# Optimization experiments

Hardware: AMD Instinct MI355X
Metric: run time of the kernel (lower is better)

Reference implementation:

```python
import jax, jax.numpy as jnp
import numpy as np

WS = 7
NHEAD = 8


def setup_inputs() -> dict:
    key = jax.random.key(0)
    k1, k2, k3 = jax.random.split(key, 3)
    B, H, W, D = 32, 56, 56, 256
    x = jax.random.normal(k1, (B, H, W, D), dtype=jnp.float32)
    in_proj_w = jax.random.normal(k2, (3 * D, D), dtype=jnp.float32) * 0.02
    in_proj_b = jnp.zeros((3 * D,), dtype=jnp.float32)
    out_w = jax.random.normal(k3, (D, D), dtype=jnp.float32) * 0.02
    out_b = jnp.zeros((D,), dtype=jnp.float32)
    return {"x": x, "in_proj_w": in_proj_w, "in_proj_b": in_proj_b,
            "out_w": out_w, "out_b": out_b}


def reference(x, in_proj_w, in_proj_b, out_w, out_b):
    B, Hf, Wf, D = x.shape
    ws = WS
    hd = D // NHEAD
    pad_h = (-Hf) % ws
    pad_w = (-Wf) % ws
    xp = jnp.pad(x, ((0, 0), (0, pad_h), (0, pad_w), (0, 0)))
    Hp, Wp = Hf + pad_h, Wf + pad_w
    nh, nw = Hp // ws, Wp // ws
    # partition into windows: [B*nh*nw, ws*ws, D]
    xw = xp.reshape(B, nh, ws, nw, ws, D).transpose(0, 1, 3, 2, 4, 5)
    xw = xw.reshape(B * nh * nw, ws * ws, D)
    N, L = xw.shape[0], ws * ws
    # qkv projection (torch MHA: x @ in_proj_w.T + in_proj_b)
    qkv = jnp.einsum('nld,ed->nle', xw, in_proj_w) + in_proj_b  # [N, L, 3D]
    q, k, v = jnp.split(qkv, 3, axis=-1)
    q = q.reshape(N, L, NHEAD, hd).transpose(0, 2, 1, 3)
    k = k.reshape(N, L, NHEAD, hd).transpose(0, 2, 1, 3)
    v = v.reshape(N, L, NHEAD, hd).transpose(0, 2, 1, 3)
    scale = 1.0 / np.sqrt(hd).astype(np.float32)
    scores = jnp.einsum('nhqd,nhkd->nhqk', q * scale, k)  # [N, H, L, L]
    attn = jax.nn.softmax(scores, axis=-1)
    o = jnp.einsum('nhqk,nhkd->nhqd', attn, v)
    o = o.transpose(0, 2, 1, 3).reshape(N, L, D)
    o = jnp.einsum('nld,ed->nle', o, out_w) + out_b
    # un-window
    o = o.reshape(B, nh, nw, ws, ws, D).transpose(0, 1, 3, 2, 4, 5)
    o = o.reshape(B, Hp, Wp, D)
    return o[:, :Hf, :Wf, :]
```

## Files before the change

kernel.cpp:

```cpp
#include <hip/hip_runtime.h>


using f16   = _Float16;
using f16x4 = __attribute__((ext_vector_type(4))) _Float16;
using f16x8 = __attribute__((ext_vector_type(8))) _Float16;
using f32x4 = __attribute__((ext_vector_type(4))) float;

#define NTOK   100352
#define DMODEL 256
#define QKVN   768
#define LDSK   72

typedef const __attribute__((address_space(1))) unsigned int* as1_u32p;
typedef __attribute__((address_space(3))) unsigned int* as3_u32p;

__device__ __forceinline__ void gload16(const void* g, void* l) {
    __builtin_amdgcn_global_load_lds((as1_u32p)g, (as3_u32p)l, 16, 0, 0);
}

__device__ __forceinline__ f16x8 zero8() {
    f16x8 z;
#pragma unroll
    for (int i = 0; i < 8; ++i) z[i] = (f16)0;
    return z;
}

#define XV4   6422528
#define WQV4  49152
__global__ __launch_bounds__(256) void convert_all(
    const float* __restrict__ X, const float* __restrict__ Wq,
    f16* __restrict__ Xh, f16* __restrict__ Wqh)
{
    const float scale = 0.17677669529663687f;
    const int total = XV4 + WQV4;
    for (int i = blockIdx.x * blockDim.x + threadIdx.x; i < total;
         i += gridDim.x * blockDim.x) {
        float4 f;
        f16x4 h;
        if (i < XV4) {
            f = reinterpret_cast<const float4*>(X)[i];
            h[0]=(f16)f.x; h[1]=(f16)f.y; h[2]=(f16)f.z; h[3]=(f16)f.w;
            reinterpret_cast<f16x4*>(Xh)[i] = h;
        } else {
            int idx = i - XV4;
            int row = idx >> 6;
            float sc = (row < 256) ? scale : 1.0f;
            f = reinterpret_cast<const float4*>(Wq)[idx];
            h[0]=(f16)(f.x*sc); h[1]=(f16)(f.y*sc); h[2]=(f16)(f.z*sc); h[3]=(f16)(f.w*sc);
            reinterpret_cast<f16x4*>(Wqh)[idx] = h;
        }
    }
}

__global__ __launch_bounds__(256) void qkv_gemm(
    const f16* __restrict__ Xh,
    const f16* __restrict__ Wh,
    const float* __restrict__ bias,
    f16* __restrict__ QKV)
{
    __shared__ f16 As[128 * 64];
    __shared__ f16 Bs[128 * 64];
    const int tid  = threadIdx.x;
    const int lane = tid & 63;
    const int wave = tid >> 6;
    int wg = blockIdx.x;
    const int cpx = (NTOK / 128) * (QKVN / 128) / 8;
    wg = (wg & 7) * cpx + (wg >> 3);
    const int m0 = (wg / (QKVN / 128)) * 128;
    const int n0 = (wg % (QKVN / 128)) * 128;
    const int wm = (wave >> 1) * 64;
    const int wn = (wave & 1) * 64;
    const int g  = lane >> 4;
    const int lr = lane & 15;

    f32x4 acc[4][4] = {};

    for (int k0 = 0; k0 < 256; k0 += 64) {
#pragma unroll
        for (int j = 0; j < 4; ++j) {
            int s   = wave * 64 + lane + j * 256;
            int row = s >> 3;
            int cs  = (s & 7) ^ (row & 7);
            gload16(Xh + (size_t)(m0 + row) * 256 + k0 + cs * 8,
                    &As[(size_t)(wave * 64 + j * 256) * 8]);
            gload16(Wh + (size_t)(n0 + row) * 256 + k0 + cs * 8,
                    &Bs[(size_t)(wave * 64 + j * 256) * 8]);
        }
        __syncthreads();
#pragma unroll
        for (int ks = 0; ks < 2; ++ks) {
            f16x8 a[4], b[4];
#pragma unroll
            for (int i = 0; i < 4; ++i) {
                int row = wm + i * 16 + lr;
                int c   = ((ks << 2) + g) ^ (row & 7);
                a[i] = *reinterpret_cast<const f16x8*>(&As[row * 64 + c * 8]);
            }
#pragma unroll
            for (int i = 0; i < 4; ++i) {
                int row = wn + i * 16 + lr;
                int c   = ((ks << 2) + g) ^ (row & 7);
                b[i] = *reinterpret_cast<const f16x8*>(&Bs[row * 64 + c * 8]);
            }
#pragma unroll
            for (int mi = 0; mi < 4; ++mi)
#pragma unroll
                for (int ni = 0; ni < 4; ++ni)
                    acc[mi][ni] = __builtin_amdgcn_mfma_f32_16x16x32_f16(a[mi], b[ni], acc[mi][ni], 0, 0, 0);
        }
        __syncthreads();
    }
    const float scale = 0.17677669529663687f;
#pragma unroll
    for (int ni = 0; ni < 4; ++ni) {
        int n = n0 + wn + ni * 16 + lr;
        float bv = bias[n];
        if (n < 256) bv *= scale;
#pragma unroll
        for (int mi = 0; mi < 4; ++mi)
#pragma unroll
            for (int r = 0; r < 4; ++r) {
                int m = m0 + wm + mi * 16 + g * 4 + r;
                QKV[(size_t)m * QKVN + n] = (f16)(acc[mi][ni][r] + bv);
            }
    }
}

__global__ __launch_bounds__(64) void win_attn(f16* __restrict__ QKV)
{
    __shared__ f16 Vt[32][LDSK];
    __shared__ f16 P[64][LDSK];
    const int lane = threadIdx.x;
    const int widx = blockIdx.x;
    const int win = widx >> 3, h = widx & 7;
    const int b = win >> 6, wh = (win >> 3) & 7, ww = win & 7;
    const int base = (b * 56 + wh * 7) * 56 + ww * 7;
    const int g = lane >> 4, lr = lane & 15;

    auto tok = [&](int row) { int rr = row / 7; return base + rr * 56 + (row - rr * 7); };

    f16x8 qf[4], kf[4];
#pragma unroll
    for (int i = 0; i < 4; ++i) {
        int row = i * 16 + lr;
        if (row < 49) {
            size_t off = (size_t)tok(row) * QKVN + h * 32 + g * 8;
            qf[i] = *reinterpret_cast<const f16x8*>(QKV + off);
            kf[i] = *reinterpret_cast<const f16x8*>(QKV + off + 256);
        } else { qf[i] = zero8(); kf[i] = zero8(); }
    }
    {
        int kk = lane;
        if (kk < 49) {
            size_t off = (size_t)tok(kk) * QKVN + 512 + h * 32;
            f16x8 vv[4];
#pragma unroll
            for (int j = 0; j < 4; ++j)
                vv[j] = *reinterpret_cast<const f16x8*>(QKV + off + j * 8);
#pragma unroll
            for (int j = 0; j < 4; ++j)
#pragma unroll
                for (int d = 0; d < 8; ++d) Vt[j * 8 + d][kk] = vv[j][d];
        } else {
#pragma unroll
            for (int d = 0; d < 32; ++d) Vt[d][kk] = (f16)0;
        }
    }
    f32x4 s[4][4] = {};
#pragma unroll
    for (int mi = 0; mi < 4; ++mi)
#pragma unroll
        for (int ni = 0; ni < 4; ++ni)
            s[mi][ni] = __builtin_amdgcn_mfma_f32_16x16x32_f16(qf[mi], kf[ni], s[mi][ni], 0, 0, 0);

    __syncthreads();
#pragma unroll
    for (int mi = 0; mi < 4; ++mi) {
#pragma unroll
        for (int r = 0; r < 4; ++r) {
            float vals[4];
            float mx = -1e30f;
#pragma unroll
            for (int ni = 0; ni < 4; ++ni) {
                int col = ni * 16 + lr;
                vals[ni] = s[mi][ni][r];
                if (col < 49) mx = fmaxf(mx, vals[ni]);
            }
#pragma unroll
            for (int d = 8; d >= 1; d >>= 1) mx = fmaxf(mx, __shfl_xor(mx, d, 64));
            float p[4], sum = 0.f;
#pragma unroll
            for (int ni = 0; ni < 4; ++ni) {
                int col = ni * 16 + lr;
                p[ni] = (col < 49) ? __expf(vals[ni] - mx) : 0.f;
                sum += p[ni];
            }
#pragma unroll
            for (int d = 8; d >= 1; d >>= 1) sum += __shfl_xor(sum, d, 64);
            float is = 1.f / sum;
            int row = mi * 16 + g * 4 + r;
#pragma unroll
            for (int ni = 0; ni < 4; ++ni)
                P[row][ni * 16 + lr] = (f16)(p[ni] * is);
        }
    }
    __syncthreads();

    f32x4 o[4][2] = {};
#pragma unroll
    for (int ks = 0; ks < 2; ++ks) {
        f16x8 pa[4], vb[2];
#pragma unroll
        for (int mi = 0; mi < 4; ++mi)
            pa[mi] = *reinterpret_cast<const f16x8*>(&P[mi * 16 + lr][ks * 32 + g * 8]);
#pragma unroll
        for (int ni = 0; ni < 2; ++ni)
            vb[ni] = *reinterpret_cast<const f16x8*>(&Vt[ni * 16 + lr][ks * 32 + g * 8]);
#pragma unroll
        for (int mi = 0; mi < 4; ++mi)
#pragma unroll
            for (int ni = 0; ni < 2; ++ni)
                o[mi][ni] = __builtin_amdgcn_mfma_f32_16x16x32_f16(pa[mi], vb[ni], o[mi][ni], 0, 0, 0);
    }
#pragma unroll
    for (int mi = 0; mi < 4; ++mi)
#pragma unroll
        for (int r = 0; r < 4; ++r) {
            int row = mi * 16 + g * 4 + r;
            if (row < 49) {
                size_t off = (size_t)tok(row) * QKVN + h * 32;
#pragma unroll
                for (int ni = 0; ni < 2; ++ni)
                    QKV[off + ni * 16 + lr] = (f16)o[mi][ni][r];
            }
        }
}

__global__ __launch_bounds__(256) void out_gemm(
    const f16* __restrict__ O,
    const float* __restrict__ W,
    const float* __restrict__ bias,
    float* __restrict__ OUT)
{
    __shared__ f16 As[128 * 64];
    __shared__ f16 Bs[128][LDSK];
    const int tid  = threadIdx.x;
    const int lane = tid & 63;
    const int wave = tid >> 6;
    int wg = blockIdx.x;
    const int cpx = (NTOK / 128) * (DMODEL / 128) / 8;
    wg = (wg & 7) * cpx + (wg >> 3);
    const int m0 = (wg / (DMODEL / 128)) * 128;
    const int n0 = (wg % (DMODEL / 128)) * 128;
    const int wm = (wave >> 1) * 64;
    const int wn = (wave & 1) * 64;
    const int g  = lane >> 4;
    const int lr = lane & 15;

    f32x4 acc[4][4] = {};

    for (int k0 = 0; k0 < 256; k0 += 64) {
#pragma unroll
        for (int j = 0; j < 4; ++j) {
            int s   = wave * 64 + lane + j * 256;
            int row = s >> 3;
            int cs  = (s & 7) ^ (row & 7);
            gload16(O + (size_t)(m0 + row) * QKVN + k0 + cs * 8,
                    &As[(size_t)(wave * 64 + j * 256) * 8]);
        }
#pragma unroll
        for (int j = 0; j < 8; ++j) {
            int v = tid + j * 256;
            int row = v >> 4, cv = v & 15;
            float4 f = *reinterpret_cast<const float4*>(W + (size_t)(n0 + row) * 256 + k0 + cv * 4);
            f16x4 h; h[0]=(f16)f.x; h[1]=(f16)f.y; h[2]=(f16)f.z; h[3]=(f16)f.w;
            *reinterpret_cast<f16x4*>(&Bs[row][cv * 4]) = h;
        }
        __syncthreads();
#pragma unroll
        for (int ks = 0; ks < 2; ++ks) {
            f16x8 a[4], b[4];
#pragma unroll
            for (int i = 0; i < 4; ++i) {
                int row = wm + i * 16 + lr;
                int c   = ((ks << 2) + g) ^ (row & 7);
                a[i] = *reinterpret_cast<const f16x8*>(&As[row * 64 + c * 8]);
            }
#pragma unroll
            for (int i = 0; i < 4; ++i)
                b[i] = *reinterpret_cast<const f16x8*>(&Bs[wn + i * 16 + lr][ks * 32 + g * 8]);
#pragma unroll
            for (int mi = 0; mi < 4; ++mi)
#pragma unroll
                for (int ni = 0; ni < 4; ++ni)
                    acc[mi][ni] = __builtin_amdgcn_mfma_f32_16x16x32_f16(a[mi], b[ni], acc[mi][ni], 0, 0, 0);
        }
        __syncthreads();
    }
#pragma unroll
    for (int ni = 0; ni < 4; ++ni) {
        int n = n0 + wn + ni * 16 + lr;
        float bv = bias[n];
#pragma unroll
        for (int mi = 0; mi < 4; ++mi)
#pragma unroll
            for (int r = 0; r < 4; ++r) {
                int m = m0 + wm + mi * 16 + g * 4 + r;
                OUT[(size_t)m * 256 + n] = acc[mi][ni][r] + bv;
            }
    }
}

extern "C" void kernel_launch(void* const* d_in, const int* in_sizes, int n_in,
                              void* d_out, int out_size, void* d_ws, size_t ws_size,
                              hipStream_t stream) {
    const float* x     = (const float*)d_in[0];
    const float* in_w  = (const float*)d_in[1];
    const float* in_b  = (const float*)d_in[2];
    const float* out_w = (const float*)d_in[3];
    const float* out_b = (const float*)d_in[4];
    float* out = (float*)d_out;
    f16* qkv = (f16*)d_ws;

    f16* xh  = (f16*)d_out;
    f16* wqh = xh + (size_t)NTOK * 256;

    convert_all<<<2048, 256, 0, stream>>>(x, in_w, xh, wqh);

    qkv_gemm<<<(NTOK / 128) * (QKVN / 128), 256, 0, stream>>>(xh, wqh, in_b, qkv);

    win_attn<<<2048 * 8, 64, 0, stream>>>(qkv);

    out_gemm<<<(NTOK / 128) * (DMODEL / 128), 256, 0, stream>>>(qkv, out_w, out_b, out);
}
```

Baseline: 178.6 us.

## Fuse window attention with output projection in one per-window kernel

Replaces the per-head attention kernel and the separate output GEMM with one kernel per window, where 8 waves each handle one head. Head outputs are staged in LDS and multiplied directly by the fp32 out-projection weights, converted to f16 on the fly. This removes the global write-back and reread of attention outputs and one kernel launch. In exchange, every block reloads and converts the weight matrix, uses a large LDS footprint that limits occupancy, and computes on padded 64-row tiles.

```diff
diff --git a/kernel.cpp b/kernel.cpp
--- a/kernel.cpp
+++ b/kernel.cpp
@@ -9,7 +9,6 @@
 #define NTOK   100352
 #define DMODEL 256
 #define QKVN   768
-#define LDSK   72
 
 typedef const __attribute__((address_space(1))) unsigned int* as1_u32p;
 typedef __attribute__((address_space(3))) unsigned int* as3_u32p;
@@ -126,13 +125,20 @@
     }
 }
 
-__global__ __launch_bounds__(64) void win_attn(f16* __restrict__ QKV)
+__global__ __launch_bounds__(512, 1) void win_attn_out(
+    const f16* __restrict__ QKV,
+    const float* __restrict__ Wo,
+    const float* __restrict__ bias,
+    float* __restrict__ OUT)
 {
-    __shared__ f16 Vt[32][LDSK];
-    __shared__ f16 P[64][LDSK];
-    const int lane = threadIdx.x;
-    const int widx = blockIdx.x;
-    const int win = widx >> 3, h = widx & 7;
+    __shared__ f16 Vt[8][32][68];
+    __shared__ f16 P[8][64][68];
+    __shared__ f16 Ol[64][260];
+
+    const int tid  = threadIdx.x;
+    const int lane = tid & 63;
+    const int h    = tid >> 6;
+    const int win  = blockIdx.x;
     const int b = win >> 6, wh = (win >> 3) & 7, ww = win & 7;
     const int base = (b * 56 + wh * 7) * 56 + ww * 7;
     const int g = lane >> 4, lr = lane & 15;
@@ -160,10 +166,10 @@
 #pragma unroll
             for (int j = 0; j < 4; ++j)
 #pragma unroll
-                for (int d = 0; d < 8; ++d) Vt[j * 8 + d][kk] = vv[j][d];
+                for (int d = 0; d < 8; ++d) Vt[h][j * 8 + d][kk] = vv[j][d];
         } else {
 #pragma unroll
-            for (int d = 0; d < 32; ++d) Vt[d][kk] = (f16)0;
+            for (int d = 0; d < 32; ++d) Vt[h][d][kk] = (f16)0;
         }
     }
     f32x4 s[4][4] = {};
@@ -201,7 +207,7 @@
             int row = mi * 16 + g * 4 + r;
 #pragma unroll
             for (int ni = 0; ni < 4; ++ni)
-                P[row][ni * 16 + lr] = (f16)(p[ni] * is);
+                P[h][row][ni * 16 + lr] = (f16)(p[ni] * is);
         }
     }
     __syncthreads();
@@ -212,10 +218,10 @@
         f16x8 pa[4], vb[2];
 #pragma unroll
         for (int mi = 0; mi < 4; ++mi)
-            pa[mi] = *reinterpret_cast<const f16x8*>(&P[mi * 16 + lr][ks * 32 + g * 8]);
+            pa[mi] = *reinterpret_cast<const f16x8*>(&P[h][mi * 16 + lr][ks * 32 + g * 8]);
 #pragma unroll
         for (int ni = 0; ni < 2; ++ni)
-            vb[ni] = *reinterpret_cast<const f16x8*>(&Vt[ni * 16 + lr][ks * 32 + g * 8]);
+            vb[ni] = *reinterpret_cast<const f16x8*>(&Vt[h][ni * 16 + lr][ks * 32 + g * 8]);
 #pragma unroll
         for (int mi = 0; mi < 4; ++mi)
 #pragma unroll
@@ -227,86 +233,46 @@
 #pragma unroll
         for (int r = 0; r < 4; ++r) {
             int row = mi * 16 + g * 4 + r;
-            if (row < 49) {
-                size_t off = (size_t)tok(row) * QKVN + h * 32;
-#pragma unroll
-                for (int ni = 0; ni < 2; ++ni)
-                    QKV[off + ni * 16 + lr] = (f16)o[mi][ni][r];
-            }
-        }
-}
-
-__global__ __launch_bounds__(256) void out_gemm(
-    const f16* __restrict__ O,
-    const float* __restrict__ W,
-    const float* __restrict__ bias,
-    float* __restrict__ OUT)
-{
-    __shared__ f16 As[128 * 64];
-    __shared__ f16 Bs[128][LDSK];
-    const int tid  = threadIdx.x;
-    const int lane = tid & 63;
-    const int wave = tid >> 6;
-    int wg = blockIdx.x;
-    const int cpx = (NTOK / 128) * (DMODEL / 128) / 8;
-    wg = (wg & 7) * cpx + (wg >> 3);
-    const int m0 = (wg / (DMODEL / 128)) * 128;
-    const int n0 = (wg % (DMODEL / 128)) * 128;
-    const int wm = (wave >> 1) * 64;
-    const int wn = (wave & 1) * 64;
-    const int g  = lane >> 4;
-    const int lr = lane & 15;
-
-    f32x4 acc[4][4] = {};
-
-    for (int k0 = 0; k0 < 256; k0 += 64) {
-#pragma unroll
-        for (int j = 0; j < 4; ++j) {
-            int s   = wave * 64 + lane + j * 256;
-            int row = s >> 3;
-            int cs  = (s & 7) ^ (row & 7);
-            gload16(O + (size_t)(m0 + row) * QKVN + k0 + cs * 8,
-                    &As[(size_t)(wave * 64 + j * 256) * 8]);
-        }
-#pragma unroll
-        for (int j = 0; j < 8; ++j) {
-            int v = tid + j * 256;
-            int row = v >> 4, cv = v & 15;
-            float4 f = *reinterpret_cast<const float4*>(W + (size_t)(n0 + row) * 256 + k0 + cv * 4);
-            f16x4 h; h[0]=(f16)f.x; h[1]=(f16)f.y; h[2]=(f16)f.z; h[3]=(f16)f.w;
-            *reinterpret_cast<f16x4*>(&Bs[row][cv * 4]) = h;
-        }
-        __syncthreads();
-#pragma unroll
-        for (int ks = 0; ks < 2; ++ks) {
-            f16x8 a[4], b[4];
-#pragma unroll
-            for (int i = 0; i < 4; ++i) {
-                int row = wm + i * 16 + lr;
-                int c   = ((ks << 2) + g) ^ (row & 7);
-                a[i] = *reinterpret_cast<const f16x8*>(&As[row * 64 + c * 8]);
-            }
-#pragma unroll
-            for (int i = 0; i < 4; ++i)
-                b[i] = *reinterpret_cast<const f16x8*>(&Bs[wn + i * 16 + lr][ks * 32 + g * 8]);
-#pragma unroll
-            for (int mi = 0; mi < 4; ++mi)
-#pragma unroll
-                for (int ni = 0; ni < 4; ++ni)
-                    acc[mi][ni] = __builtin_amdgcn_mfma_f32_16x16x32_f16(a[mi], b[ni], acc[mi][ni], 0, 0, 0);
-        }
-        __syncthreads();
-    }
-#pragma unroll
-    for (int ni = 0; ni < 4; ++ni) {
-        int n = n0 + wn + ni * 16 + lr;
+#pragma unroll
+            for (int ni = 0; ni < 2; ++ni)
+                Ol[row][h * 32 + ni * 16 + lr] = (f16)o[mi][ni][r];
+        }
+    __syncthreads();
+
+    const int n0 = h * 32;
+    f32x4 acc[4][2] = {};
+    for (int k0 = 0; k0 < 256; k0 += 32) {
+        f16x8 a[4], bfr[2];
+#pragma unroll
+        for (int i = 0; i < 4; ++i)
+            a[i] = *reinterpret_cast<const f16x8*>(&Ol[i * 16 + lr][k0 + g * 8]);
+#pragma unroll
+        for (int ni = 0; ni < 2; ++ni) {
+            const float* wrow = Wo + (size_t)(n0 + ni * 16 + lr) * 256 + k0 + g * 8;
+            float4 f0 = *reinterpret_cast<const float4*>(wrow);
+            float4 f1 = *reinterpret_cast<const float4*>(wrow + 4);
+            f16x8 hh;
+            hh[0]=(f16)f0.x; hh[1]=(f16)f0.y; hh[2]=(f16)f0.z; hh[3]=(f16)f0.w;
+            hh[4]=(f16)f1.x; hh[5]=(f16)f1.y; hh[6]=(f16)f1.z; hh[7]=(f16)f1.w;
+            bfr[ni] = hh;
+        }
+#pragma unroll
+        for (int mi = 0; mi < 4; ++mi)
+#pragma unroll
+            for (int ni = 0; ni < 2; ++ni)
+                acc[mi][ni] = __builtin_amdgcn_mfma_f32_16x16x32_f16(a[mi], bfr[ni], acc[mi][ni], 0, 0, 0);
+    }
+#pragma unroll
+    for (int ni = 0; ni < 2; ++ni) {
+        int n = n0 + ni * 16 + lr;
         float bv = bias[n];
 #pragma unroll
         for (int mi = 0; mi < 4; ++mi)
 #pragma unroll
             for (int r = 0; r < 4; ++r) {
-                int m = m0 + wm + mi * 16 + g * 4 + r;
-                OUT[(size_t)m * 256 + n] = acc[mi][ni][r] + bv;
+                int m = mi * 16 + g * 4 + r;
+                if (m < 49)
+                    OUT[(size_t)tok(m) * 256 + n] = acc[mi][ni][r] + bv;
             }
     }
 }
@@ -329,7 +295,5 @@
 
     qkv_gemm<<<(NTOK / 128) * (QKVN / 128), 256, 0, stream>>>(xh, wqh, in_b, qkv);
 
-    win_attn<<<2048 * 8, 64, 0, stream>>>(qkv);
-
-    out_gemm<<<(NTOK / 128) * (DMODEL / 128), 256, 0, stream>>>(qkv, out_w, out_b, out);
-}
+    win_attn_out<<<2048, 512, 0, stream>>>(qkv, out_w, out_b, out);
+}
```

After: 229.7 us. +28.6%, slower.
